# Kernel tuning notes

Measured on AMD Instinct MI355X. Metric: run time of the kernel, lower is better.

The kernel has to match this reference:

```python
import jax, jax.numpy as jnp
import numpy as np

D_MODEL = 1024
N_HEADS = 16
D_K = D_MODEL // N_HEADS
MAX_SEQ = 2048
THETA = 10000.0


def _make_cos_sin():
    # cos_sin[i, k, 0] = cos(i / theta**(2k/d_k)), [.., 1] = sin(...)
    pos = np.arange(MAX_SEQ, dtype=np.float32)[:, None]
    k = np.arange(D_K // 2, dtype=np.float32)[None, :]
    ang = pos / (THETA ** (2.0 * k / D_K))
    return jnp.asarray(np.stack([np.cos(ang), np.sin(ang)], axis=-1), dtype=jnp.float32)


def setup_inputs() -> dict:
    key = jax.random.key(0)
    ks = jax.random.split(key, 5)
    std = 2.0 / (D_MODEL + D_MODEL)
    def w(k):
        return std * jax.random.truncated_normal(k, -3.0, 3.0, (D_MODEL, D_MODEL), dtype=jnp.float32)
    return {
        "x": jax.random.normal(ks[0], (4, 2048, D_MODEL), dtype=jnp.float32),
        "Wq": w(ks[1]),
        "Wk": w(ks[2]),
        "Wv": w(ks[3]),
        "Wo": w(ks[4]),
        "cos_sin": _make_cos_sin(),
        "token_positions": jnp.arange(2048, dtype=jnp.int32),
    }


def _rope(x, cos_sin, pos):
    # x: [B, H, S, d_k]; rotate consecutive pairs
    B, H, S, d = x.shape
    xt = x.reshape(B, H, S, d // 2, 2)
    cos = cos_sin[pos, :, 0]  # [S, d/2]
    sin = cos_sin[pos, :, 1]
    x0, x1 = xt[..., 0], xt[..., 1]
    r0 = cos * x0 - sin * x1
    r1 = sin * x0 + cos * x1
    return jnp.stack([r0, r1], axis=-1).reshape(B, H, S, d)


def reference(x, Wq, Wk, Wv, Wo, cos_sin, token_positions):
    B, S, D = x.shape
    H, d = N_HEADS, D_K
    def proj(W):
        y = jnp.einsum('bsi,oi->bso', x, W)
        return y.reshape(B, S, H, d).transpose(0, 2, 1, 3)  # [B,H,S,d]
    q = _rope(proj(Wq), cos_sin, token_positions)
    k = _rope(proj(Wk), cos_sin, token_positions)
    v = proj(Wv)
    scores = jnp.einsum('bhqd,bhkd->bhqk', q, k) / jnp.sqrt(jnp.float32(d))
    causal = jnp.tril(jnp.ones((S, S), dtype=bool))
    scores = jnp.where(causal, scores, -jnp.inf)
    attn = jax.nn.softmax(scores, axis=-1)
    out = jnp.einsum('bhqk,bhkd->bhqd', attn, v)
    out = out.transpose(0, 2, 1, 3).reshape(B, S, D)
    return jnp.einsum('bsi,oi->bso', out, Wo)
```

## Files before the change

kernel.cpp:

```cpp
#include <hip/hip_runtime.h>

constexpr int B_  = 4;
constexpr int S_  = 2048;
constexpr int D_  = 1024;
constexpr int H_  = 16;
constexpr int DK_ = 64;
constexpr int M_  = B_ * S_;

typedef __attribute__((ext_vector_type(8))) short short8;
typedef __attribute__((ext_vector_type(4))) float f32x4;
typedef __attribute__((ext_vector_type(4))) unsigned short us4;

__device__ __forceinline__ unsigned short f2b(float f) {
  unsigned int u = __float_as_uint(f);
  u += 0x7FFFu + ((u >> 16) & 1u);
  return (unsigned short)(u >> 16);
}
__device__ __forceinline__ float b2f(unsigned short h) {
  return __uint_as_float(((unsigned int)h) << 16);
}

#define GLOAD16(g, l) __builtin_amdgcn_global_load_lds( \
    (const __attribute__((address_space(1))) unsigned int*)(g), \
    (__attribute__((address_space(3))) unsigned int*)(l), 16, 0, 0)

__global__ __launch_bounds__(256) void conv_kernel(
    const float* __restrict__ x,
    const float* __restrict__ wq, const float* __restrict__ wk, const float* __restrict__ wv,
    unsigned short* __restrict__ xb, unsigned short* __restrict__ wb)
{
  const int NX4 = (M_ * D_) / 4;
  const int NW4 = (3 * D_ * D_) / 4;
  int stride = gridDim.x * blockDim.x;
  for (int i = blockIdx.x * blockDim.x + threadIdx.x; i < NX4 + NW4; i += stride) {
    const float4* src; unsigned short* dst; int o;
    if (i < NX4) { src = (const float4*)x; dst = xb; o = i; }
    else {
      int wi = i - NX4;
      int mat = wi >> 18;
      o = wi & 262143;
      src = (const float4*)(mat == 0 ? wq : (mat == 1 ? wk : wv));
      dst = wb + mat * (D_ * D_);
    }
    float4 v = src[o];
    us4 r; r.x = f2b(v.x); r.y = f2b(v.y); r.z = f2b(v.z); r.w = f2b(v.w);
    *(us4*)(dst + o * 4) = r;
  }
}

__global__ __launch_bounds__(256) void conv_wo_kernel(
    const float* __restrict__ wo, unsigned short* __restrict__ wob)
{
  int i = blockIdx.x * 256 + threadIdx.x;
  float4 v = ((const float4*)wo)[i];
  us4 r; r.x = f2b(v.x); r.y = f2b(v.y); r.z = f2b(v.z); r.w = f2b(v.w);
  *(us4*)(wob + i * 4) = r;
}

__global__ __launch_bounds__(256) void gemm_qkv_kernel(
    const unsigned short* __restrict__ xb,
    const unsigned short* __restrict__ wb,
    const float* __restrict__ cs,
    const int* __restrict__ pos,
    unsigned short* __restrict__ qb,
    unsigned short* __restrict__ kb,
    unsigned short* __restrict__ vtb)
{
  __shared__ unsigned short As[128 * 32];
  __shared__ unsigned short Bs[128 * 32];
  const int tid  = threadIdx.x;
  const int lane = tid & 63;
  const int wid  = tid >> 6;
  const int wm = wid >> 1, wn = wid & 1;
  const int m0 = blockIdx.x * 128;
  const int n0 = blockIdx.y * 128;
  const int l15 = lane & 15, l4 = lane >> 4;

  const int c0 = tid;
  const int rA0 = c0 >> 2, cA0 = (c0 & 3) * 8;
  const int c1 = tid + 256;
  const int rA1 = c1 >> 2, cA1 = (c1 & 3) * 8;
  const int lb0 = (wid * 64) * 8;
  const int lb1 = (256 + wid * 64) * 8;

  f32x4 acc[4][4] = {};

  for (int t = 0; t < 32; ++t) {
    __syncthreads();
    GLOAD16(xb + (m0 + rA0) * D_ + t * 32 + cA0, &As[lb0]);
    GLOAD16(xb + (m0 + rA1) * D_ + t * 32 + cA1, &As[lb1]);
    GLOAD16(wb + (n0 + rA0) * D_ + t * 32 + cA0, &Bs[lb0]);
    GLOAD16(wb + (n0 + rA1) * D_ + t * 32 + cA1, &Bs[lb1]);
    __syncthreads();

    short8 af[4], bfr[4];
    #pragma unroll
    for (int mi = 0; mi < 4; ++mi) af[mi]  = *(const short8*)&As[(wm*64 + mi*16 + l15)*32 + l4*8];
    #pragma unroll
    for (int ni = 0; ni < 4; ++ni) bfr[ni] = *(const short8*)&Bs[(wn*64 + ni*16 + l15)*32 + l4*8];
    __builtin_amdgcn_s_setprio(1);
    #pragma unroll
    for (int mi = 0; mi < 4; ++mi)
      #pragma unroll
      for (int ni = 0; ni < 4; ++ni)
        acc[mi][ni] = __builtin_amdgcn_mfma_f32_16x16x32_bf16(af[mi], bfr[ni], acc[mi][ni], 0, 0, 0);
    __builtin_amdgcn_s_setprio(0);
  }

  const int bidx = m0 >> 11;
  const int sbase = (m0 & 2047) + wm * 64;

  if (n0 < 2048) {
    unsigned short* dst = (n0 < 1024) ? qb : kb;
    const int nn0 = n0 & 1023;
    const float2* cs2 = (const float2*)cs;
    const float sg = (l15 & 1) ? 1.0f : -1.0f;
    #pragma unroll
    for (int mi = 0; mi < 4; ++mi)
      #pragma unroll
      for (int j = 0; j < 4; ++j) {
        int s = sbase + mi*16 + l4*4 + j;
        int p = pos[s];
        #pragma unroll
        for (int ni = 0; ni < 4; ++ni) {
          int col = nn0 + wn*64 + ni*16 + l15;
          int h = col >> 6, dd = col & 63;
          float val = acc[mi][ni][j];
          float par = __shfl_xor(val, 1);
          float2 cv = cs2[p*32 + (dd >> 1)];
          float r = fmaf(cv.x, val, sg * cv.y * par);
          dst[((bidx*H_ + h)*S_ + s)*DK_ + dd] = f2b(r);
        }
      }
  } else {
    const int nn0 = n0 & 1023;
    #pragma unroll
    for (int mi = 0; mi < 4; ++mi)
      #pragma unroll
      for (int ni = 0; ni < 4; ++ni)
        #pragma unroll
        for (int j = 0; j < 4; ++j) {
          int s = sbase + mi*16 + l4*4 + j;
          int col = nn0 + wn*64 + ni*16 + l15;
          int h = col >> 6, dd = col & 63;
          vtb[((bidx*H_ + h)*DK_ + dd)*S_ + s] = f2b(acc[mi][ni][j]);
        }
  }
}

__global__ __launch_bounds__(256, 2) void attn_kernel(
    const unsigned short* __restrict__ qb,
    const unsigned short* __restrict__ kb,
    const unsigned short* __restrict__ vtb,
    unsigned short* __restrict__ ao)
{
  __shared__ unsigned short Ks[64][72];
  __shared__ unsigned short Vs[64][72];
  __shared__ unsigned short Ps[4][2][16][72];
  const int tid = threadIdx.x, lane = tid & 63, wid = tid >> 6;
  const int l15 = lane & 15, l4 = lane >> 4;

  const int id  = blockIdx.x;
  const int swz = (id & 7) * 64 + (id >> 3);
  const int bh  = swz >> 3;
  const int qpair = swz & 7;

  const unsigned short* qp = qb  + bh * S_ * DK_;
  const unsigned short* kp = kb  + bh * S_ * DK_;
  const unsigned short* vp = vtb + bh * DK_ * S_;
  const int bidx = bh >> 4, h = bh & 15;

  for (int half = 0; half < 2; ++half) {
    const int qt = half ? (15 - qpair) : qpair;
    const int q0 = qt * 128;
    const int nkt = 2 * qt + 2;

    short8 kv[2], vv[2];
    #pragma unroll
    for (int jj = 0; jj < 2; ++jj) {
      int c = tid + jj * 256;
      int r = c >> 3, col = (c & 7) * 8;
      kv[jj] = *(const short8*)(kp + r*DK_ + col);
      vv[jj] = *(const short8*)(vp + r*S_ + col);
    }

    short8 qf[2][2];
    #pragma unroll
    for (int y = 0; y < 2; ++y)
      #pragma unroll
      for (int kbk = 0; kbk < 2; ++kbk) {
        short8 raw = *(const short8*)(qp + (q0 + y*64 + wid*16 + l15)*DK_ + kbk*32 + l4*8);
        #pragma unroll
        for (int i = 0; i < 8; ++i) {
          float f = b2f((unsigned short)raw[i]) * 0.125f;
          raw[i] = (short)f2b(f);
        }
        qf[y][kbk] = raw;
      }

    f32x4 oacc[2][4] = {};
    float mrun[2] = {-1e30f, -1e30f}, lrun[2] = {0.0f, 0.0f};

    for (int kt = 0; kt < nkt; ++kt) {
      __syncthreads();
      #pragma unroll
      for (int jj = 0; jj < 2; ++jj) {
        int c = tid + jj * 256;
        int r = c >> 3, col = (c & 7) * 8;
        *(short8*)&Ks[r][col] = kv[jj];
        *(short8*)&Vs[r][col] = vv[jj];
      }
      __syncthreads();

      if (kt + 1 < nkt) {
        #pragma unroll
        for (int jj = 0; jj < 2; ++jj) {
          int c = tid + jj * 256;
          int r = c >> 3, col = (c & 7) * 8;
          kv[jj] = *(const short8*)(kp + ((kt+1)*64 + r)*DK_ + col);
          vv[jj] = *(const short8*)(vp + r*S_ + (kt+1)*64 + col);
        }
      }

      #pragma unroll
      for (int y = 0; y < 2; ++y) {
        if (kt > 2*qt + y) continue;

        f32x4 sc[4];
        __builtin_amdgcn_s_setprio(1);
        #pragma unroll
        for (int nb = 0; nb < 4; ++nb) {
          short8 k0 = *(const short8*)&Ks[nb*16 + l15][l4*8];
          short8 k1 = *(const short8*)&Ks[nb*16 + l15][32 + l4*8];
          f32x4 z = {};
          z = __builtin_amdgcn_mfma_f32_16x16x32_bf16(k0, qf[y][0], z, 0, 0, 0);
          z = __builtin_amdgcn_mfma_f32_16x16x32_bf16(k1, qf[y][1], z, 0, 0, 0);
          sc[nb] = z;
        }
        __builtin_amdgcn_s_setprio(0);

        if (kt == 2*qt + y) {
          const int qg = q0 + y*64 + wid*16 + l15;
          #pragma unroll
          for (int nb = 0; nb < 4; ++nb)
            #pragma unroll
            for (int j = 0; j < 4; ++j) {
              int kg = kt*64 + nb*16 + l4*4 + j;
              if (kg > qg) sc[nb][j] = -1e30f;
            }
        }

        float tm = sc[0][0];
        #pragma unroll
        for (int nb = 0; nb < 4; ++nb)
          #pragma unroll
          for (int j = 0; j < 4; ++j) tm = fmaxf(tm, sc[nb][j]);
        tm = fmaxf(tm, __shfl_xor(tm, 16));
        tm = fmaxf(tm, __shfl_xor(tm, 32));
        if (!__all(tm - mrun[y] <= 8.0f)) {
          float mnew = fmaxf(mrun[y], tm);
          float corr = __expf(mrun[y] - mnew);
          mrun[y] = mnew;
          lrun[y] *= corr;
          #pragma unroll
          for (int j = 0; j < 4; ++j) {
            float cj = __shfl(corr, l4*4 + j);
            #pragma unroll
            for (int nb = 0; nb < 4; ++nb) oacc[y][nb][j] *= cj;
          }
        }
        float rs = 0.0f;
        #pragma unroll
        for (int nb = 0; nb < 4; ++nb)
          #pragma unroll
          for (int j = 0; j < 4; ++j) {
            float p = __expf(sc[nb][j] - mrun[y]);
            sc[nb][j] = p;
            rs += p;
          }
        rs += __shfl_xor(rs, 16);
        rs += __shfl_xor(rs, 32);
        lrun[y] += rs;

        #pragma unroll
        for (int nb = 0; nb < 4; ++nb) {
          uint2 w;
          w.x = (unsigned int)f2b(sc[nb][0]) | ((unsigned int)f2b(sc[nb][1]) << 16);
          w.y = (unsigned int)f2b(sc[nb][2]) | ((unsigned int)f2b(sc[nb][3]) << 16);
          *(uint2*)&Ps[wid][y][l15][nb*16 + l4*4] = w;
        }
        asm volatile("s_waitcnt lgkmcnt(0)" ::: "memory");
        short8 pa0 = *(const short8*)&Ps[wid][y][l15][l4*8];
        short8 pa1 = *(const short8*)&Ps[wid][y][l15][32 + l4*8];

        __builtin_amdgcn_s_setprio(1);
        #pragma unroll
        for (int nb = 0; nb < 4; ++nb) {
          short8 v0 = *(const short8*)&Vs[nb*16 + l15][l4*8];
          short8 v1 = *(const short8*)&Vs[nb*16 + l15][32 + l4*8];
          oacc[y][nb] = __builtin_amdgcn_mfma_f32_16x16x32_bf16(pa0, v0, oacc[y][nb], 0, 0, 0);
          oacc[y][nb] = __builtin_amdgcn_mfma_f32_16x16x32_bf16(pa1, v1, oacc[y][nb], 0, 0, 0);
        }
        __builtin_amdgcn_s_setprio(0);
      }
    }

    #pragma unroll
    for (int y = 0; y < 2; ++y)
      #pragma unroll
      for (int j = 0; j < 4; ++j) {
        float lj = __shfl(lrun[y], l4*4 + j);
        float inv = 1.0f / lj;
        int row = q0 + y*64 + wid*16 + l4*4 + j;
        #pragma unroll
        for (int nb = 0; nb < 4; ++nb) {
          int dim = nb*16 + l15;
          ao[((bidx*S_ + row)*H_ + h)*DK_ + dim] = f2b(oacc[y][nb][j] * inv);
        }
      }
  }
}

__global__ __launch_bounds__(256) void gemm_out_kernel(
    const unsigned short* __restrict__ ao,
    const unsigned short* __restrict__ wob,
    float* __restrict__ out)
{
  __shared__ unsigned short As[128 * 32];
  __shared__ unsigned short Bs[128 * 32];
  const int tid = threadIdx.x, lane = tid & 63, wid = tid >> 6;
  const int wm = wid >> 1, wn = wid & 1;
  const int m0 = blockIdx.x * 128, n0 = blockIdx.y * 128;
  const int l15 = lane & 15, l4 = lane >> 4;

  const int c0 = tid;
  const int rA0 = c0 >> 2, cA0 = (c0 & 3) * 8;
  const int c1 = tid + 256;
  const int rA1 = c1 >> 2, cA1 = (c1 & 3) * 8;
  const int lb0 = (wid * 64) * 8;
  const int lb1 = (256 + wid * 64) * 8;

  f32x4 acc[4][4] = {};

  for (int t = 0; t < 32; ++t) {
    __syncthreads();
    GLOAD16(ao  + (m0 + rA0) * D_ + t * 32 + cA0, &As[lb0]);
    GLOAD16(ao  + (m0 + rA1) * D_ + t * 32 + cA1, &As[lb1]);
    GLOAD16(wob + (n0 + rA0) * D_ + t * 32 + cA0, &Bs[lb0]);
    GLOAD16(wob + (n0 + rA1) * D_ + t * 32 + cA1, &Bs[lb1]);
    __syncthreads();

    short8 af[4], bfr[4];
    #pragma unroll
    for (int mi = 0; mi < 4; ++mi) af[mi]  = *(const short8*)&As[(wm*64 + mi*16 + l15)*32 + l4*8];
    #pragma unroll
    for (int ni = 0; ni < 4; ++ni) bfr[ni] = *(const short8*)&Bs[(wn*64 + ni*16 + l15)*32 + l4*8];
    __builtin_amdgcn_s_setprio(1);
    #pragma unroll
    for (int mi = 0; mi < 4; ++mi)
      #pragma unroll
      for (int ni = 0; ni < 4; ++ni)
        acc[mi][ni] = __builtin_amdgcn_mfma_f32_16x16x32_bf16(af[mi], bfr[ni], acc[mi][ni], 0, 0, 0);
    __builtin_amdgcn_s_setprio(0);
  }

  #pragma unroll
  for (int mi = 0; mi < 4; ++mi)
    #pragma unroll
    for (int ni = 0; ni < 4; ++ni)
      #pragma unroll
      for (int j = 0; j < 4; ++j) {
        int row = m0 + wm*64 + mi*16 + l4*4 + j;
        int col = n0 + wn*64 + ni*16 + l15;
        out[row * D_ + col] = acc[mi][ni][j];
      }
}

extern "C" void kernel_launch(void* const* d_in, const int* in_sizes, int n_in,
                              void* d_out, int out_size, void* d_ws, size_t ws_size,
                              hipStream_t stream)
{
  const float* x  = (const float*)d_in[0];
  const float* wq = (const float*)d_in[1];
  const float* wk = (const float*)d_in[2];
  const float* wv = (const float*)d_in[3];
  const float* wo = (const float*)d_in[4];
  const float* cs = (const float*)d_in[5];
  const int*  pos = (const int*)d_in[6];
  float* out = (float*)d_out;

  unsigned short* xb = (unsigned short*)d_out;
  unsigned short* wb = xb + M_ * D_;

  unsigned short* qb  = (unsigned short*)d_ws;
  unsigned short* kbf = qb  + M_ * D_;
  unsigned short* vtb = kbf + M_ * D_;
  unsigned short* aob = vtb + M_ * D_;
  unsigned short* wob = qb;

  conv_kernel<<<dim3(2048), dim3(256), 0, stream>>>(x, wq, wk, wv, xb, wb);
  gemm_qkv_kernel<<<dim3(64, 24), dim3(256), 0, stream>>>(xb, wb, cs, pos, qb, kbf, vtb);
  attn_kernel<<<dim3(512), dim3(256), 0, stream>>>(qb, kbf, vtb, aob);
  conv_wo_kernel<<<dim3(1024), dim3(256), 0, stream>>>(wo, wob);
  gemm_out_kernel<<<dim3(64, 8), dim3(256), 0, stream>>>(aob, wob, out);

  (void)in_sizes; (void)n_in; (void)out_size; (void)ws_size;
}
```

Before: 205.9 us.

## Split attention into one block per q-tile, use exp2 softmax and packed bf16 stores

```diff
diff --git a/kernel.cpp b/kernel.cpp
--- a/kernel.cpp
+++ b/kernel.cpp
@@ -18,6 +18,16 @@
 }
 __device__ __forceinline__ float b2f(unsigned short h) {
   return __uint_as_float(((unsigned int)h) << 16);
+}
+__device__ __forceinline__ unsigned int cvtpk(float lo, float hi) {
+  unsigned int w;
+  asm("v_cvt_pk_bf16_f32 %0, %1, %2" : "=v"(w) : "v"(lo), "v"(hi));
+  return w;
+}
+__device__ __forceinline__ float exp2v(float x) {
+  float r;
+  asm("v_exp_f32 %0, %1" : "=v"(r) : "v"(x));
+  return r;
 }
 
 #define GLOAD16(g, l) __builtin_amdgcn_global_load_lds( \
@@ -134,21 +144,23 @@
       }
   } else {
     const int nn0 = n0 & 1023;
-    #pragma unroll
-    for (int mi = 0; mi < 4; ++mi)
-      #pragma unroll
-      for (int ni = 0; ni < 4; ++ni)
-        #pragma unroll
-        for (int j = 0; j < 4; ++j) {
-          int s = sbase + mi*16 + l4*4 + j;
-          int col = nn0 + wn*64 + ni*16 + l15;
-          int h = col >> 6, dd = col & 63;
-          vtb[((bidx*H_ + h)*DK_ + dd)*S_ + s] = f2b(acc[mi][ni][j]);
-        }
-  }
-}
-
-__global__ __launch_bounds__(256, 2) void attn_kernel(
+    const int hB = (nn0 + wn*64) >> 6;
+    #pragma unroll
+    for (int mi = 0; mi < 4; ++mi) {
+      int s4 = sbase + mi*16 + l4*4;
+      #pragma unroll
+      for (int ni = 0; ni < 4; ++ni) {
+        int dd = ni*16 + l15;
+        uint2 w;
+        w.x = cvtpk(acc[mi][ni][0], acc[mi][ni][1]);
+        w.y = cvtpk(acc[mi][ni][2], acc[mi][ni][3]);
+        *(uint2*)(vtb + ((bidx*H_ + hB)*DK_ + dd)*S_ + s4) = w;
+      }
+    }
+  }
+}
+
+__global__ __launch_bounds__(256, 4) void attn_kernel(
     const unsigned short* __restrict__ qb,
     const unsigned short* __restrict__ kb,
     const unsigned short* __restrict__ vtb,
@@ -156,169 +168,166 @@
 {
   __shared__ unsigned short Ks[64][72];
   __shared__ unsigned short Vs[64][72];
-  __shared__ unsigned short Ps[4][2][16][72];
+  __shared__ unsigned short Ps[4][16][72];
   const int tid = threadIdx.x, lane = tid & 63, wid = tid >> 6;
   const int l15 = lane & 15, l4 = lane >> 4;
 
   const int id  = blockIdx.x;
-  const int swz = (id & 7) * 64 + (id >> 3);
-  const int bh  = swz >> 3;
-  const int qpair = swz & 7;
+  const int xcd = id & 7, jj2 = id >> 3;
+  const int bh  = xcd * 8 + (jj2 & 7);
+  const int qt  = 15 - (jj2 >> 3);
+  const int q0  = qt * 128;
+  const int nkt = 2 * qt + 2;
 
   const unsigned short* qp = qb  + bh * S_ * DK_;
   const unsigned short* kp = kb  + bh * S_ * DK_;
   const unsigned short* vp = vtb + bh * DK_ * S_;
   const int bidx = bh >> 4, h = bh & 15;
 
-  for (int half = 0; half < 2; ++half) {
-    const int qt = half ? (15 - qpair) : qpair;
-    const int q0 = qt * 128;
-    const int nkt = 2 * qt + 2;
-
-    short8 kv[2], vv[2];
+  const float QSC = 0.18033688f;
+  short8 qf[2][2];
+  #pragma unroll
+  for (int y = 0; y < 2; ++y)
+    #pragma unroll
+    for (int kbk = 0; kbk < 2; ++kbk) {
+      short8 raw = *(const short8*)(qp + (q0 + y*64 + wid*16 + l15)*DK_ + kbk*32 + l4*8);
+      #pragma unroll
+      for (int i = 0; i < 8; ++i) {
+        float f = b2f((unsigned short)raw[i]) * QSC;
+        raw[i] = (short)f2b(f);
+      }
+      qf[y][kbk] = raw;
+    }
+
+  f32x4 oacc[2][4] = {};
+  float mrun[2] = {-1e30f, -1e30f}, lrun[2] = {0.0f, 0.0f};
+
+  short8 kv[2], vv[2];
+  #pragma unroll
+  for (int jj = 0; jj < 2; ++jj) {
+    int c = tid + jj * 256;
+    int r = c >> 3, col = (c & 7) * 8;
+    kv[jj] = *(const short8*)(kp + r*DK_ + col);
+    vv[jj] = *(const short8*)(vp + r*S_ + col);
+  }
+
+  for (int kt = 0; kt < nkt; ++kt) {
+    __syncthreads();
     #pragma unroll
     for (int jj = 0; jj < 2; ++jj) {
       int c = tid + jj * 256;
       int r = c >> 3, col = (c & 7) * 8;
-      kv[jj] = *(const short8*)(kp + r*DK_ + col);
-      vv[jj] = *(const short8*)(vp + r*S_ + col);
-    }
-
-    short8 qf[2][2];
-    #pragma unroll
-    for (int y = 0; y < 2; ++y)
-      #pragma unroll
-      for (int kbk = 0; kbk < 2; ++kbk) {
-        short8 raw = *(const short8*)(qp + (q0 + y*64 + wid*16 + l15)*DK_ + kbk*32 + l4*8);
-        #pragma unroll
-        for (int i = 0; i < 8; ++i) {
-          float f = b2f((unsigned short)raw[i]) * 0.125f;
-          raw[i] = (short)f2b(f);
-        }
-        qf[y][kbk] = raw;
-      }
-
-    f32x4 oacc[2][4] = {};
-    float mrun[2] = {-1e30f, -1e30f}, lrun[2] = {0.0f, 0.0f};
-
-    for (int kt = 0; kt < nkt; ++kt) {
-      __syncthreads();
+      *(short8*)&Ks[r][col] = kv[jj];
+      *(short8*)&Vs[r][col] = vv[jj];
+    }
+    __syncthreads();
+
+    if (kt + 1 < nkt) {
       #pragma unroll
       for (int jj = 0; jj < 2; ++jj) {
         int c = tid + jj * 256;
         int r = c >> 3, col = (c & 7) * 8;
-        *(short8*)&Ks[r][col] = kv[jj];
-        *(short8*)&Vs[r][col] = vv[jj];
-      }
-      __syncthreads();
-
-      if (kt + 1 < nkt) {
-        #pragma unroll
-        for (int jj = 0; jj < 2; ++jj) {
-          int c = tid + jj * 256;
-          int r = c >> 3, col = (c & 7) * 8;
-          kv[jj] = *(const short8*)(kp + ((kt+1)*64 + r)*DK_ + col);
-          vv[jj] = *(const short8*)(vp + r*S_ + (kt+1)*64 + col);
-        }
-      }
-
-      #pragma unroll
-      for (int y = 0; y < 2; ++y) {
-        if (kt > 2*qt + y) continue;
-
-        f32x4 sc[4];
-        __builtin_amdgcn_s_setprio(1);
-        #pragma unroll
-        for (int nb = 0; nb < 4; ++nb) {
-          short8 k0 = *(const short8*)&Ks[nb*16 + l15][l4*8];
-          short8 k1 = *(const short8*)&Ks[nb*16 + l15][32 + l4*8];
-          f32x4 z = {};
-          z = __builtin_amdgcn_mfma_f32_16x16x32_bf16(k0, qf[y][0], z, 0, 0, 0);
-          z = __builtin_amdgcn_mfma_f32_16x16x32_bf16(k1, qf[y][1], z, 0, 0, 0);
-          sc[nb] = z;
-        }
-        __builtin_amdgcn_s_setprio(0);
-
-        if (kt == 2*qt + y) {
-          const int qg = q0 + y*64 + wid*16 + l15;
-          #pragma unroll
-          for (int nb = 0; nb < 4; ++nb)
-            #pragma unroll
-            for (int j = 0; j < 4; ++j) {
-              int kg = kt*64 + nb*16 + l4*4 + j;
-              if (kg > qg) sc[nb][j] = -1e30f;
-            }
-        }
-
-        float tm = sc[0][0];
-        #pragma unroll
-        for (int nb = 0; nb < 4; ++nb)
-          #pragma unroll
-          for (int j = 0; j < 4; ++j) tm = fmaxf(tm, sc[nb][j]);
-        tm = fmaxf(tm, __shfl_xor(tm, 16));
-        tm = fmaxf(tm, __shfl_xor(tm, 32));
-        if (!__all(tm - mrun[y] <= 8.0f)) {
-          float mnew = fmaxf(mrun[y], tm);
-          float corr = __expf(mrun[y] - mnew);
-          mrun[y] = mnew;
-          lrun[y] *= corr;
-          #pragma unroll
-          for (int j = 0; j < 4; ++j) {
-            float cj = __shfl(corr, l4*4 + j);
-            #pragma unroll
-            for (int nb = 0; nb < 4; ++nb) oacc[y][nb][j] *= cj;
-          }
-        }
-        float rs = 0.0f;
+        kv[jj] = *(const short8*)(kp + ((kt+1)*64 + r)*DK_ + col);
+        vv[jj] = *(const short8*)(vp + r*S_ + (kt+1)*64 + col);
+      }
+    }
+
+    #pragma unroll
+    for (int y = 0; y < 2; ++y) {
+      if (kt > 2*qt + y) continue;
+
+      f32x4 sc[4];
+      __builtin_amdgcn_s_setprio(1);
+      #pragma unroll
+      for (int nb = 0; nb < 4; ++nb) {
+        short8 k0 = *(const short8*)&Ks[nb*16 + l15][l4*8];
+        short8 k1 = *(const short8*)&Ks[nb*16 + l15][32 + l4*8];
+        f32x4 z = {};
+        z = __builtin_amdgcn_mfma_f32_16x16x32_bf16(k0, qf[y][0], z, 0, 0, 0);
+        z = __builtin_amdgcn_mfma_f32_16x16x32_bf16(k1, qf[y][1], z, 0, 0, 0);
+        sc[nb] = z;
+      }
+      __builtin_amdgcn_s_setprio(0);
+
+      if (kt == 2*qt + y) {
+        const int qg = q0 + y*64 + wid*16 + l15;
         #pragma unroll
         for (int nb = 0; nb < 4; ++nb)
           #pragma unroll
           for (int j = 0; j < 4; ++j) {
-            float p = __expf(sc[nb][j] - mrun[y]);
-            sc[nb][j] = p;
-            rs += p;
+            int kg = kt*64 + nb*16 + l4*4 + j;
+            if (kg > qg) sc[nb][j] = -1e30f;
           }
-        rs += __shfl_xor(rs, 16);
-        rs += __shfl_xor(rs, 32);
-        lrun[y] += rs;
-
+      }
+
+      float tm = sc[0][0];
+      #pragma unroll
+      for (int nb = 0; nb < 4; ++nb)
         #pragma unroll
-        for (int nb = 0; nb < 4; ++nb) {
-          uint2 w;
-          w.x = (unsigned int)f2b(sc[nb][0]) | ((unsigned int)f2b(sc[nb][1]) << 16);
-          w.y = (unsigned int)f2b(sc[nb][2]) | ((unsigned int)f2b(sc[nb][3]) << 16);
-          *(uint2*)&Ps[wid][y][l15][nb*16 + l4*4] = w;
+        for (int j = 0; j < 4; ++j) tm = fmaxf(tm, sc[nb][j]);
+      tm = fmaxf(tm, __shfl_xor(tm, 16));
+      tm = fmaxf(tm, __shfl_xor(tm, 32));
+      if (!__all(tm - mrun[y] <= 8.0f)) {
+        float mnew = fmaxf(mrun[y], tm);
+        float corr = exp2v(mrun[y] - mnew);
+        mrun[y] = mnew;
+        lrun[y] *= corr;
+        #pragma unroll
+        for (int j = 0; j < 4; ++j) {
+          float cj = __shfl(corr, l4*4 + j);
+          #pragma unroll
+          for (int nb = 0; nb < 4; ++nb) oacc[y][nb][j] *= cj;
         }
-        asm volatile("s_waitcnt lgkmcnt(0)" ::: "memory");
-        short8 pa0 = *(const short8*)&Ps[wid][y][l15][l4*8];
-        short8 pa1 = *(const short8*)&Ps[wid][y][l15][32 + l4*8];
-
-        __builtin_amdgcn_s_setprio(1);
+      }
+      float rs = 0.0f;
+      #pragma unroll
+      for (int nb = 0; nb < 4; ++nb)
         #pragma unroll
-        for (int nb = 0; nb < 4; ++nb) {
-          short8 v0 = *(const short8*)&Vs[nb*16 + l15][l4*8];
-          short8 v1 = *(const short8*)&Vs[nb*16 + l15][32 + l4*8];
-          oacc[y][nb] = __builtin_amdgcn_mfma_f32_16x16x32_bf16(pa0, v0, oacc[y][nb], 0, 0, 0);
-          oacc[y][nb] = __builtin_amdgcn_mfma_f32_16x16x32_bf16(pa1, v1, oacc[y][nb], 0, 0, 0);
+        for (int j = 0; j < 4; ++j) {
+          float p = exp2v(sc[nb][j] - mrun[y]);
+          sc[nb][j] = p;
+          rs += p;
         }
-        __builtin_amdgcn_s_setprio(0);
-      }
-    }
-
-    #pragma unroll
-    for (int y = 0; y < 2; ++y)
-      #pragma unroll
-      for (int j = 0; j < 4; ++j) {
-        float lj = __shfl(lrun[y], l4*4 + j);
-        float inv = 1.0f / lj;
-        int row = q0 + y*64 + wid*16 + l4*4 + j;
-        #pragma unroll
-        for (int nb = 0; nb < 4; ++nb) {
-          int dim = nb*16 + l15;
-          ao[((bidx*S_ + row)*H_ + h)*DK_ + dim] = f2b(oacc[y][nb][j] * inv);
-        }
-      }
-  }
+      rs += __shfl_xor(rs, 16);
+      rs += __shfl_xor(rs, 32);
+      lrun[y] += rs;
+
+      #pragma unroll
+      for (int nb = 0; nb < 4; ++nb) {
+        uint2 w;
+        w.x = cvtpk(sc[nb][0], sc[nb][1]);
+        w.y = cvtpk(sc[nb][2], sc[nb][3]);
+        *(uint2*)&Ps[wid][l15][nb*16 + l4*4] = w;
+      }
+      asm volatile("s_waitcnt lgkmcnt(0)" ::: "memory");
+      short8 pa0 = *(const short8*)&Ps[wid][l15][l4*8];
+      short8 pa1 = *(const short8*)&Ps[wid][l15][32 + l4*8];
+
+      __builtin_amdgcn_s_setprio(1);
+      #pragma unroll
+      for (int nb = 0; nb < 4; ++nb) {
+        short8 v0 = *(const short8*)&Vs[nb*16 + l15][l4*8];
+        short8 v1 = *(const short8*)&Vs[nb*16 + l15][32 + l4*8];
+        oacc[y][nb] = __builtin_amdgcn_mfma_f32_16x16x32_bf16(pa0, v0, oacc[y][nb], 0, 0, 0);
+        oacc[y][nb] = __builtin_amdgcn_mfma_f32_16x16x32_bf16(pa1, v1, oacc[y][nb], 0, 0, 0);
+      }
+      __builtin_amdgcn_s_setprio(0);
+    }
+  }
+
+  #pragma unroll
+  for (int y = 0; y < 2; ++y)
+    #pragma unroll
+    for (int j = 0; j < 4; ++j) {
+      float lj = __shfl(lrun[y], l4*4 + j);
+      float inv = 1.0f / lj;
+      int row = q0 + y*64 + wid*16 + l4*4 + j;
+      #pragma unroll
+      for (int nb = 0; nb < 4; ++nb) {
+        int dim = nb*16 + l15;
+        ao[((bidx*S_ + row)*H_ + h)*DK_ + dim] = f2b(oacc[y][nb][j] * inv);
+      }
+    }
 }
 
 __global__ __launch_bounds__(256) void gemm_out_kernel(
@@ -400,7 +409,7 @@
 
   conv_kernel<<<dim3(2048), dim3(256), 0, stream>>>(x, wq, wk, wv, xb, wb);
   gemm_qkv_kernel<<<dim3(64, 24), dim3(256), 0, stream>>>(xb, wb, cs, pos, qb, kbf, vtb);
-  attn_kernel<<<dim3(512), dim3(256), 0, stream>>>(qb, kbf, vtb, aob);
+  attn_kernel<<<dim3(1024), dim3(256), 0, stream>>>(qb, kbf, vtb, aob);
   conv_wo_kernel<<<dim3(1024), dim3(256), 0, stream>>>(wo, wob);
   gemm_out_kernel<<<dim3(64, 8), dim3(256), 0, stream>>>(aob, wob, out);
 
```

Result: no change. 201.9 us (-1.9%).
